# Kernel tuning notes

Measured on AMD Instinct MI355X. Metric: run time of the kernel, lower is better.

The kernel has to match this reference:

```python
import jax, jax.numpy as jnp
import numpy as np

B, D, H, O = 8192, 1024, 1024, 1024
LN_EPS = 1e-6  # flax LayerNorm default


def setup_inputs() -> dict:
    key = jax.random.key(0)
    ks = jax.random.split(key, 18)
    s_i = 1.0 / np.sqrt(D)  # lecun_normal-ish scale, fan_in = D
    s_h = 1.0 / np.sqrt(H)
    inp = {
        "x": jax.random.normal(ks[0], (B, D), jnp.float32),
        "h": jax.random.normal(ks[1], (B, H), jnp.float32),
        # input projections (use_bias=True)
        "Wir": jax.random.normal(ks[2], (D, H), jnp.float32) * s_i,
        "bir": jax.random.normal(ks[3], (H,), jnp.float32) * 0.01,
        "Wiz": jax.random.normal(ks[4], (D, H), jnp.float32) * s_i,
        "biz": jnp.zeros((H,), jnp.float32),  # chrono_init with T_min=None -> zeros
        "Win": jax.random.normal(ks[5], (D, H), jnp.float32) * s_i,
        "bin_": jax.random.normal(ks[6], (H,), jnp.float32) * 0.01,
        # hidden projections (hr, hz: no bias; hn: bias)
        "Whr": jax.random.normal(ks[7], (H, H), jnp.float32) * s_h,
        "Whz": jax.random.normal(ks[8], (H, H), jnp.float32) * s_h,
        "Whn": jax.random.normal(ks[9], (H, H), jnp.float32) * s_h,
        "bhn": jax.random.normal(ks[10], (H,), jnp.float32) * 0.01,
        # LayerNorm params
        "ln_scale": jnp.ones((H,), jnp.float32),
        "ln_bias": jnp.zeros((H,), jnp.float32),
        # readout
        "Wout": jax.random.normal(ks[11], (H, O), jnp.float32) * s_h,
        "bout": jax.random.normal(ks[12], (O,), jnp.float32) * 0.01,
    }
    return inp


def _layer_norm(x, scale, bias):
    mu = jnp.mean(x, axis=-1, keepdims=True)
    var = jnp.mean(jnp.square(x - mu), axis=-1, keepdims=True)
    return (x - mu) * jax.lax.rsqrt(var + LN_EPS) * scale + bias


def reference(x, h, Wir, bir, Wiz, biz, Win, bin_, Whr, Whz, Whn, bhn,
              ln_scale, ln_bias, Wout, bout):
    # GRU recurrence (stop_gradients='none' branch)
    r = jax.nn.sigmoid(x @ Wir + bir + h @ Whr)          # [B,H]
    z = jax.nn.sigmoid(x @ Wiz + biz + h @ Whz)          # [B,H]
    n = jnp.tanh(x @ Win + bin_ + r * (h @ Whn + bhn))   # [B,H]
    new_h = (1.0 - z) * n + z * h                        # [B,H]
    # readout: LayerNorm then Dense
    out = _layer_norm(new_h, ln_scale, ln_bias) @ Wout + bout  # [B,O]
    return new_h, out
```

## Files before the change

kernel.cpp:

```cpp
#include <hip/hip_runtime.h>
#include <math.h>

#define B_ 8192
#define H_ 1024
#define K2 2048

typedef __attribute__((ext_vector_type(8))) short bf16x8;
typedef __attribute__((ext_vector_type(4))) float f32x4;
typedef unsigned short u16;

__device__ __forceinline__ u16 f2bf(float f) {
  unsigned u = __float_as_uint(f);
  u += 0x7fffu + ((u >> 16) & 1u);
  return (u16)(u >> 16);
}
__device__ __forceinline__ float bf2f(u16 s) { return __uint_as_float(((unsigned)s) << 16); }

__global__ __launch_bounds__(256) void split_hl(const float* __restrict__ src,
                                                u16* __restrict__ hi, u16* __restrict__ lo,
                                                int col04) {
  const int n4 = B_ * H_ / 4;
  int i = blockIdx.x * blockDim.x + threadIdx.x;
  int stride = gridDim.x * blockDim.x;
  for (; i < n4; i += stride) {
    float4 v = reinterpret_cast<const float4*>(src)[i];
    int row = i >> 8;
    int c4 = i & 255;
    float c[4] = {v.x, v.y, v.z, v.w};
    u16 hh[4], ll[4];
#pragma unroll
    for (int j = 0; j < 4; j++) {
      hh[j] = f2bf(c[j]);
      ll[j] = f2bf(c[j] - bf2f(hh[j]));
    }
    ushort4 h4 = {hh[0], hh[1], hh[2], hh[3]};
    ushort4 l4 = {ll[0], ll[1], ll[2], ll[3]};
    size_t o4 = (size_t)row * (K2 / 4) + col04 + c4;
    reinterpret_cast<ushort4*>(hi)[o4] = h4;
    reinterpret_cast<ushort4*>(lo)[o4] = l4;
  }
}

__global__ __launch_bounds__(256) void transpose_split(const float* __restrict__ W,
                                                       u16* __restrict__ Thi,
                                                       u16* __restrict__ Tlo,
                                                       int K, int N, int ldo, int koff) {
  __shared__ float tile[32][33];
  int bx = blockIdx.x * 32;
  int by = blockIdx.y * 32;
  int tx = threadIdx.x, ty = threadIdx.y;
#pragma unroll
  for (int i = 0; i < 4; i++)
    tile[ty + i * 8][tx] = W[(size_t)(by + ty + i * 8) * N + bx + tx];
  __syncthreads();
#pragma unroll
  for (int i = 0; i < 4; i++) {
    float v = tile[tx][ty + i * 8];
    u16 hv = f2bf(v);
    u16 lv = f2bf(v - bf2f(hv));
    size_t o = (size_t)(bx + ty + i * 8) * ldo + koff + by + tx;
    Thi[o] = hv;
    Tlo[o] = lv;
  }
}

#define BM 128
#define BN 128
#define BK 64

__device__ __forceinline__ void gload16(const void* g, void* l) {
  __builtin_amdgcn_global_load_lds((const __attribute__((address_space(1))) unsigned int*)g,
                                   (__attribute__((address_space(3))) unsigned int*)l,
                                   16, 0, 0);
}

__global__ __launch_bounds__(256, 2) void gemm3(const u16* __restrict__ Ahi,
                                                const u16* __restrict__ Alo, int lda,
                                                const u16* __restrict__ Bhi,
                                                const u16* __restrict__ Blo,
                                                const float* __restrict__ bias, float* C,
                                                int N, int K, int mode,
                                                const float* zbuf, const float* xnbuf,
                                                const float* hnbuf, const float* hbuf) {
  __shared__ u16 lds[4 * BM * BK];
  u16* sAh = lds;
  u16* sAl = lds + BM * BK;
  u16* sBh = lds + 2 * BM * BK;
  u16* sBl = lds + 3 * BM * BK;

  const int tid = threadIdx.x;
  const int lane = tid & 63;
  const int wv = tid >> 6;
  const int wr = wv >> 1, wc = wv & 1;
  const int fr = lane & 15;
  const int fs = lane >> 4;

  const int lin = blockIdx.y * gridDim.x + blockIdx.x;
  const int cpx = (gridDim.x * gridDim.y) >> 3;
  const int nlin = (lin & 7) * cpx + (lin >> 3);
  const int m0 = (nlin / gridDim.x) * BM;
  const int n0 = (nlin % gridDim.x) * BN;

  f32x4 acc[4][4] = {};

  for (int k0 = 0; k0 < K; k0 += BK) {
#pragma unroll
    for (int q = 0; q < 4; q++) {
      int idx = q * 256 + tid;
      int row = idx >> 3;
      int ls = (idx & 7) ^ (row & 7);
      size_t ga = (size_t)(m0 + row) * lda + k0 + ls * 8;
      size_t gb = (size_t)(n0 + row) * K + k0 + ls * 8;
      gload16(Ahi + ga, sAh + (size_t)idx * 8);
      gload16(Alo + ga, sAl + (size_t)idx * 8);
      gload16(Bhi + gb, sBh + (size_t)idx * 8);
      gload16(Blo + gb, sBl + (size_t)idx * 8);
    }
    __syncthreads();

#pragma unroll
    for (int kh = 0; kh < 2; kh++) {
      bf16x8 ah[4], al[4], bh[4], bl[4];
#pragma unroll
      for (int i = 0; i < 4; i++) {
        int ar = wr * 64 + i * 16 + fr;
        int ao = ar * 64 + (((kh * 4 + fs) ^ (ar & 7)) << 3);
        ah[i] = *reinterpret_cast<const bf16x8*>(sAh + ao);
        al[i] = *reinterpret_cast<const bf16x8*>(sAl + ao);
        int br = wc * 64 + i * 16 + fr;
        int bo = br * 64 + (((kh * 4 + fs) ^ (br & 7)) << 3);
        bh[i] = *reinterpret_cast<const bf16x8*>(sBh + bo);
        bl[i] = *reinterpret_cast<const bf16x8*>(sBl + bo);
      }
#pragma unroll
      for (int mi = 0; mi < 4; mi++)
#pragma unroll
        for (int ni = 0; ni < 4; ni++) {
          acc[mi][ni] = __builtin_amdgcn_mfma_f32_16x16x32_bf16(ah[mi], bh[ni], acc[mi][ni], 0, 0, 0);
          acc[mi][ni] = __builtin_amdgcn_mfma_f32_16x16x32_bf16(al[mi], bh[ni], acc[mi][ni], 0, 0, 0);
          acc[mi][ni] = __builtin_amdgcn_mfma_f32_16x16x32_bf16(ah[mi], bl[ni], acc[mi][ni], 0, 0, 0);
        }
    }
    __syncthreads();
  }

#pragma unroll
  for (int mi = 0; mi < 4; mi++) {
    int grow = m0 + wr * 64 + mi * 16 + fs * 4;
#pragma unroll
    for (int ni = 0; ni < 4; ni++) {
      int gcol = n0 + wc * 64 + ni * 16 + fr;
      float bv = bias[gcol];
      if (mode == 0) {
#pragma unroll
        for (int j = 0; j < 4; j++)
          C[(size_t)(grow + j) * N + gcol] = acc[mi][ni][j] + bv;
      } else {
#pragma unroll
        for (int j = 0; j < 4; j++) {
          size_t idx = (size_t)(grow + j) * N + gcol;
          float z = 1.f / (1.f + expf(-zbuf[idx]));
          float r = 1.f / (1.f + expf(-(acc[mi][ni][j] + bv)));
          float n = tanhf(xnbuf[idx] + r * hnbuf[idx]);
          C[idx] = (1.f - z) * n + z * hbuf[idx];
        }
      }
    }
  }
}

__global__ __launch_bounds__(256) void ln_split(const float* __restrict__ src,
                                                const float* __restrict__ scale,
                                                const float* __restrict__ bias,
                                                u16* __restrict__ lhi, u16* __restrict__ llo) {
  int row = blockIdx.x, t = threadIdx.x;
  float4 vv = reinterpret_cast<const float4*>(src + (size_t)row * H_)[t];
  float v[4] = {vv.x, vv.y, vv.z, vv.w};
  float s = 0.f, s2 = 0.f;
#pragma unroll
  for (int i = 0; i < 4; i++) {
    s += v[i];
    s2 += v[i] * v[i];
  }
#pragma unroll
  for (int m = 32; m >= 1; m >>= 1) {
    s += __shfl_xor(s, m);
    s2 += __shfl_xor(s2, m);
  }
  __shared__ float red[8];
  int lane = t & 63, wv = t >> 6;
  if (lane == 0) {
    red[wv] = s;
    red[4 + wv] = s2;
  }
  __syncthreads();
  s = red[0] + red[1] + red[2] + red[3];
  s2 = red[4] + red[5] + red[6] + red[7];
  float mu = s * (1.f / H_);
  float var = s2 * (1.f / H_) - mu * mu;
  float inv = rsqrtf(var + 1e-6f);
  float4 sc = reinterpret_cast<const float4*>(scale)[t];
  float4 bi = reinterpret_cast<const float4*>(bias)[t];
  float scv[4] = {sc.x, sc.y, sc.z, sc.w};
  float biv[4] = {bi.x, bi.y, bi.z, bi.w};
  u16 hh[4], ll[4];
#pragma unroll
  for (int i = 0; i < 4; i++) {
    float y = (v[i] - mu) * inv * scv[i] + biv[i];
    hh[i] = f2bf(y);
    ll[i] = f2bf(y - bf2f(hh[i]));
  }
  ushort4 h4 = {hh[0], hh[1], hh[2], hh[3]};
  ushort4 l4 = {ll[0], ll[1], ll[2], ll[3]};
  reinterpret_cast<ushort4*>(lhi)[(size_t)row * 256 + t] = h4;
  reinterpret_cast<ushort4*>(llo)[(size_t)row * 256 + t] = l4;
}

extern "C" void kernel_launch(void* const* d_in, const int* in_sizes, int n_in,
                              void* d_out, int out_size, void* d_ws, size_t ws_size,
                              hipStream_t stream) {
  const float* x = (const float*)d_in[0];
  const float* h = (const float*)d_in[1];
  const float* Wir = (const float*)d_in[2];
  const float* bir = (const float*)d_in[3];
  const float* Wiz = (const float*)d_in[4];
  const float* biz = (const float*)d_in[5];
  const float* Win = (const float*)d_in[6];
  const float* bin_ = (const float*)d_in[7];
  const float* Whr = (const float*)d_in[8];
  const float* Whz = (const float*)d_in[9];
  const float* Whn = (const float*)d_in[10];
  const float* bhn = (const float*)d_in[11];
  const float* ln_scale = (const float*)d_in[12];
  const float* ln_bias = (const float*)d_in[13];
  const float* Wout = (const float*)d_in[14];
  const float* bout = (const float*)d_in[15];

  float* out_h = (float*)d_out;
  float* out_o = (float*)d_out + (size_t)B_ * H_;

  char* ws = (char*)d_ws;
  size_t off = 0;
  auto alloc = [&](size_t bytes) {
    void* p = ws + off;
    off += (bytes + 255) & ~(size_t)255;
    return p;
  };
  u16* xh_hi = (u16*)alloc((size_t)B_ * K2 * 2);
  u16* xh_lo = (u16*)alloc((size_t)B_ * K2 * 2);
  u16* WrT_hi = (u16*)alloc((size_t)H_ * K2 * 2);
  u16* WrT_lo = (u16*)alloc((size_t)H_ * K2 * 2);
  u16* WzT_hi = (u16*)alloc((size_t)H_ * K2 * 2);
  u16* WzT_lo = (u16*)alloc((size_t)H_ * K2 * 2);
  u16* WinT_hi = (u16*)alloc((size_t)H_ * H_ * 2);
  u16* WinT_lo = (u16*)alloc((size_t)H_ * H_ * 2);
  u16* WhnT_hi = (u16*)alloc((size_t)H_ * H_ * 2);
  u16* WhnT_lo = (u16*)alloc((size_t)H_ * H_ * 2);
  u16* WoT_hi = (u16*)alloc((size_t)H_ * H_ * 2);
  u16* WoT_lo = (u16*)alloc((size_t)H_ * H_ * 2);
  float* HN = (float*)alloc((size_t)B_ * H_ * 4);
  u16* ln_hi = xh_hi;
  u16* ln_lo = xh_lo;

  split_hl<<<2048, 256, 0, stream>>>(x, xh_hi, xh_lo, 0);
  split_hl<<<2048, 256, 0, stream>>>(h, xh_hi, xh_lo, 256);

  dim3 tb(32, 8), tg(H_ / 32, H_ / 32);
  transpose_split<<<tg, tb, 0, stream>>>(Wir, WrT_hi, WrT_lo, H_, H_, K2, 0);
  transpose_split<<<tg, tb, 0, stream>>>(Whr, WrT_hi, WrT_lo, H_, H_, K2, 1024);
  transpose_split<<<tg, tb, 0, stream>>>(Wiz, WzT_hi, WzT_lo, H_, H_, K2, 0);
  transpose_split<<<tg, tb, 0, stream>>>(Whz, WzT_hi, WzT_lo, H_, H_, K2, 1024);
  transpose_split<<<tg, tb, 0, stream>>>(Win, WinT_hi, WinT_lo, H_, H_, H_, 0);
  transpose_split<<<tg, tb, 0, stream>>>(Whn, WhnT_hi, WhnT_lo, H_, H_, H_, 0);
  transpose_split<<<tg, tb, 0, stream>>>(Wout, WoT_hi, WoT_lo, H_, H_, H_, 0);

  dim3 gg(H_ / BN, B_ / BM);
  gemm3<<<gg, 256, 0, stream>>>(xh_hi, xh_lo, K2, WzT_hi, WzT_lo, biz, out_h, H_, K2, 0,
                                nullptr, nullptr, nullptr, nullptr);
  gemm3<<<gg, 256, 0, stream>>>(xh_hi, xh_lo, K2, WinT_hi, WinT_lo, bin_, out_o, H_, H_, 0,
                                nullptr, nullptr, nullptr, nullptr);
  gemm3<<<gg, 256, 0, stream>>>(xh_hi + H_, xh_lo + H_, K2, WhnT_hi, WhnT_lo, bhn, HN, H_, H_, 0,
                                nullptr, nullptr, nullptr, nullptr);
  gemm3<<<gg, 256, 0, stream>>>(xh_hi, xh_lo, K2, WrT_hi, WrT_lo, bir, out_h, H_, K2, 1,
                                out_h, out_o, HN, h);
  ln_split<<<B_, 256, 0, stream>>>(out_h, ln_scale, ln_bias, ln_hi, ln_lo);
  gemm3<<<gg, 256, 0, stream>>>(ln_hi, ln_lo, H_, WoT_hi, WoT_lo, bout, out_o, H_, H_, 0,
                                nullptr, nullptr, nullptr, nullptr);
}
```

Baseline: 541.8 us.

## Double-buffer GEMM LDS tiles with BK=32 and interleaved hi/lo layout

Replaces the single-buffered BK=64 main loop with a two-stage LDS ping-pong at BK=32. Each buffer interleaves hi and lo bf16 chunks per row, and global-to-LDS loads for tile t+2 are issued right after fragments for tile t are read. The intent is to hide global load latency behind the 3xMFMA compute, using explicit vmcnt waits, raw s_barrier and setprio. Halving BK doubles the number of barriers per K, and the hand-managed waitcnt sequencing is fragile.

Measured after the change: 588.3 us. +8.6%, slower.

```diff
diff --git a/kernel.cpp b/kernel.cpp
--- a/kernel.cpp
+++ b/kernel.cpp
@@ -66,7 +66,7 @@
 
 #define BM 128
 #define BN 128
-#define BK 64
+#define BK 32
 
 __device__ __forceinline__ void gload16(const void* g, void* l) {
   __builtin_amdgcn_global_load_lds((const __attribute__((address_space(1))) unsigned int*)g,
@@ -82,11 +82,7 @@
                                                 int N, int K, int mode,
                                                 const float* zbuf, const float* xnbuf,
                                                 const float* hnbuf, const float* hbuf) {
-  __shared__ u16 lds[4 * BM * BK];
-  u16* sAh = lds;
-  u16* sAl = lds + BM * BK;
-  u16* sBh = lds + 2 * BM * BK;
-  u16* sBl = lds + 3 * BM * BK;
+  __shared__ u16 lds[2][2 * BM * 2 * BK];
 
   const int tid = threadIdx.x;
   const int lane = tid & 63;
@@ -101,47 +97,86 @@
   const int m0 = (nlin / gridDim.x) * BM;
   const int n0 = (nlin % gridDim.x) * BN;
 
+  const u16* gp[8];
+  int ldsoff[8];
+#pragma unroll
+  for (int q = 0; q < 8; q++) {
+    int idx = q * 256 + tid;
+    int isB = idx >> 10;
+    int r = (idx >> 3) & 127;
+    int l = (idx & 7) ^ (r & 7);
+    int seg = l >> 1, hl = l & 1;
+    const u16* hiP = isB ? Bhi : Ahi;
+    const u16* loP = isB ? Blo : Alo;
+    size_t row_ld = isB ? (size_t)K : (size_t)lda;
+    int row0 = isB ? n0 : m0;
+    gp[q] = (hl ? loP : hiP) + (size_t)(row0 + r) * row_ld + seg * 8;
+    ldsoff[q] = idx * 8;
+  }
+
+  int oah[4], oal[4], obh[4], obl[4];
+#pragma unroll
+  for (int i = 0; i < 4; i++) {
+    int ar = wr * 64 + i * 16 + fr;
+    oah[i] = ar * 64 + ((((fs << 1)) ^ (ar & 7)) << 3);
+    oal[i] = ar * 64 + ((((fs << 1) | 1) ^ (ar & 7)) << 3);
+    int br = wc * 64 + i * 16 + fr;
+    obh[i] = 2 * BM * BK + br * 64 + ((((fs << 1)) ^ (br & 7)) << 3);
+    obl[i] = 2 * BM * BK + br * 64 + ((((fs << 1) | 1) ^ (br & 7)) << 3);
+  }
+
   f32x4 acc[4][4] = {};
-
-  for (int k0 = 0; k0 < K; k0 += BK) {
-#pragma unroll
-    for (int q = 0; q < 4; q++) {
-      int idx = q * 256 + tid;
-      int row = idx >> 3;
-      int ls = (idx & 7) ^ (row & 7);
-      size_t ga = (size_t)(m0 + row) * lda + k0 + ls * 8;
-      size_t gb = (size_t)(n0 + row) * K + k0 + ls * 8;
-      gload16(Ahi + ga, sAh + (size_t)idx * 8);
-      gload16(Alo + ga, sAl + (size_t)idx * 8);
-      gload16(Bhi + gb, sBh + (size_t)idx * 8);
-      gload16(Blo + gb, sBl + (size_t)idx * 8);
-    }
-    __syncthreads();
-
-#pragma unroll
-    for (int kh = 0; kh < 2; kh++) {
-      bf16x8 ah[4], al[4], bh[4], bl[4];
-#pragma unroll
-      for (int i = 0; i < 4; i++) {
-        int ar = wr * 64 + i * 16 + fr;
-        int ao = ar * 64 + (((kh * 4 + fs) ^ (ar & 7)) << 3);
-        ah[i] = *reinterpret_cast<const bf16x8*>(sAh + ao);
-        al[i] = *reinterpret_cast<const bf16x8*>(sAl + ao);
-        int br = wc * 64 + i * 16 + fr;
-        int bo = br * 64 + (((kh * 4 + fs) ^ (br & 7)) << 3);
-        bh[i] = *reinterpret_cast<const bf16x8*>(sBh + bo);
-        bl[i] = *reinterpret_cast<const bf16x8*>(sBl + bo);
+  const int nt = K / BK;
+
+  auto stage = [&](int b) {
+#pragma unroll
+    for (int q = 0; q < 8; q++) {
+      gload16(gp[q], &lds[b][0] + ldsoff[q]);
+      gp[q] += BK;
+    }
+  };
+
+  stage(0);
+  stage(1);
+  asm volatile("s_waitcnt vmcnt(8)" ::: "memory");
+  __builtin_amdgcn_sched_barrier(0);
+  __builtin_amdgcn_s_barrier();
+
+  for (int t = 0; t < nt; ++t) {
+    const int b = t & 1;
+    const u16* sT = &lds[b][0];
+    bf16x8 ah[4], al[4], bh[4], bl[4];
+#pragma unroll
+    for (int i = 0; i < 4; i++) {
+      ah[i] = *reinterpret_cast<const bf16x8*>(sT + oah[i]);
+      al[i] = *reinterpret_cast<const bf16x8*>(sT + oal[i]);
+      bh[i] = *reinterpret_cast<const bf16x8*>(sT + obh[i]);
+      bl[i] = *reinterpret_cast<const bf16x8*>(sT + obl[i]);
+    }
+    asm volatile("s_waitcnt lgkmcnt(0)" ::: "memory");
+    __builtin_amdgcn_sched_barrier(0);
+    __builtin_amdgcn_s_barrier();
+    if (t + 2 < nt) stage(b);
+
+    __builtin_amdgcn_s_setprio(1);
+#pragma unroll
+    for (int mi = 0; mi < 4; mi++)
+#pragma unroll
+      for (int ni = 0; ni < 4; ni++) {
+        acc[mi][ni] = __builtin_amdgcn_mfma_f32_16x16x32_bf16(ah[mi], bh[ni], acc[mi][ni], 0, 0, 0);
+        acc[mi][ni] = __builtin_amdgcn_mfma_f32_16x16x32_bf16(al[mi], bh[ni], acc[mi][ni], 0, 0, 0);
+        acc[mi][ni] = __builtin_amdgcn_mfma_f32_16x16x32_bf16(ah[mi], bl[ni], acc[mi][ni], 0, 0, 0);
       }
-#pragma unroll
-      for (int mi = 0; mi < 4; mi++)
-#pragma unroll
-        for (int ni = 0; ni < 4; ni++) {
-          acc[mi][ni] = __builtin_amdgcn_mfma_f32_16x16x32_bf16(ah[mi], bh[ni], acc[mi][ni], 0, 0, 0);
-          acc[mi][ni] = __builtin_amdgcn_mfma_f32_16x16x32_bf16(al[mi], bh[ni], acc[mi][ni], 0, 0, 0);
-          acc[mi][ni] = __builtin_amdgcn_mfma_f32_16x16x32_bf16(ah[mi], bl[ni], acc[mi][ni], 0, 0, 0);
-        }
-    }
-    __syncthreads();
+    __builtin_amdgcn_s_setprio(0);
+    __builtin_amdgcn_sched_barrier(0);
+
+    if (t + 2 < nt) {
+      asm volatile("s_waitcnt vmcnt(8)" ::: "memory");
+    } else if (t + 1 < nt) {
+      asm volatile("s_waitcnt vmcnt(0)" ::: "memory");
+    }
+    __builtin_amdgcn_sched_barrier(0);
+    if (t + 1 < nt) __builtin_amdgcn_s_barrier();
   }
 
 #pragma unroll
```
